# Optimization experiments

Hardware: AMD Instinct MI355X
Metric: run time of the kernel (lower is better)

Reference implementation:

```python
import jax, jax.numpy as jnp
import numpy as np

NUM_HEADS = 8


def setup_inputs() -> dict:
    key = jax.random.key(0)
    ks = jax.random.split(key, 7)
    B, C, L = 4, 512, 2048
    s = 1.0 / np.sqrt(C)
    return {
        "x": jax.random.normal(ks[0], (B, C, L), dtype=jnp.float32),
        "wq": jax.random.normal(ks[1], (C, C), dtype=jnp.float32) * s,
        "bq": jax.random.normal(ks[2], (C,), dtype=jnp.float32) * 0.01,
        "wk": jax.random.normal(ks[3], (C, C), dtype=jnp.float32) * s,
        "bk": jax.random.normal(ks[4], (C,), dtype=jnp.float32) * 0.01,
        "wv": jax.random.normal(ks[5], (C, C), dtype=jnp.float32) * s,
        "bv": jax.random.normal(ks[6], (C,), dtype=jnp.float32) * 0.01,
    }


def reference(x, wq, bq, wk, bk, wv, bv):
    B, C, L = x.shape
    H = NUM_HEADS
    Ch = C // H

    def proj(w, b):
        # 1x1 Conv1d == per-position channel GEMM: (B,C,L) x (O,C) -> (B,O,L)
        return jnp.einsum('bcl,oc->bol', x, w) + b[None, :, None]

    q = proj(wq, bq).reshape(B, H, Ch, L)
    k = proj(wk, bk).reshape(B, H, Ch, L)
    v = proj(wv, bv).reshape(B, H, Ch, L)

    # q^T k over channel dim -> (B,H,L,L)
    scale = 1.0 / jnp.sqrt(jnp.asarray(Ch, dtype=x.dtype))
    scores = jnp.einsum('bhcl,bhcm->bhlm', q, k) * scale
    attn = jax.nn.softmax(scores, axis=-1)

    # FAITHFUL quirk: torch code uses .view (reshape), NOT transpose, on v
    v2 = v.reshape(B, H, L, Ch)
    out = jnp.einsum('bhlm,bhmc->bhlc', attn, v2)
    # and .view back to (B, C, L) — again a plain reshape
    return out.reshape(B, C, L)
```

## Files before the change

### kernel.cpp

```cpp
#include <hip/hip_runtime.h>


typedef unsigned short u16;
typedef unsigned int   u32;
typedef short bf16x8 __attribute__((ext_vector_type(8)));
typedef u16  u16x8  __attribute__((ext_vector_type(8)));
typedef float f32x16 __attribute__((ext_vector_type(16)));

#define SCALE_Q 0.18033688011112042f

__device__ __forceinline__ u16 f2b(float f) {
    u32 u = __float_as_uint(f);
    u += 0x7FFFu + ((u >> 16) & 1u);
    return (u16)(u >> 16);
}

__device__ __forceinline__ float exp2_(float x) {
#if __has_builtin(__builtin_amdgcn_exp2f)
    return __builtin_amdgcn_exp2f(x);
#else
    return exp2f(x);
#endif
}

__device__ __forceinline__ u32 cvtpk(float lo, float hi) {
    u32 d;
    asm("v_cvt_pk_bf16_f32 %0, %1, %2" : "=v"(d) : "v"(lo), "v"(hi));
    return d;
}

__device__ __forceinline__ void pl32swap(u32& a, u32& b) {
    asm volatile("v_permlane32_swap_b32 %0, %1" : "+v"(a), "+v"(b));
}

__device__ __forceinline__ void g2l16(const u16* g, u16* l) {
    __builtin_amdgcn_global_load_lds(
        (const __attribute__((address_space(1))) unsigned int*)g,
        (__attribute__((address_space(3))) unsigned int*)l, 16, 0, 0);
}

#define WAITV(N) asm volatile("s_waitcnt vmcnt(" #N ")" ::: "memory")
#define WAITL0   asm volatile("s_waitcnt lgkmcnt(0)" ::: "memory")
#define SBAR     __builtin_amdgcn_s_barrier()
#define SCHED0   __builtin_amdgcn_sched_barrier(0)

__global__ __launch_bounds__(256) void prep_kernel(
    const float* __restrict__ wq, const float* __restrict__ wk,
    const float* __restrict__ wv, const float* __restrict__ x,
    u16* __restrict__ wcat, u16* __restrict__ xT)
{
    const int bid = blockIdx.x, t = threadIdx.x;
    if (bid < 384) {
        int e0 = bid * 2048 + t * 8;
        const float* src = (e0 < 262144) ? wq : (e0 < 524288) ? wk : wv;
        int eo = e0 & 262143;
        float4 a = *(const float4*)(src + eo);
        float4 b = *(const float4*)(src + eo + 4);
        u16x8 o;
        o[0]=f2b(a.x); o[1]=f2b(a.y); o[2]=f2b(a.z); o[3]=f2b(a.w);
        o[4]=f2b(b.x); o[5]=f2b(b.y); o[6]=f2b(b.z); o[7]=f2b(b.w);
        *(u16x8*)(wcat + e0) = o;
        return;
    }
    int xb = bid - 384;
    int b = xb >> 8, ct = (xb >> 5) & 7, lt = xb & 31;
    __shared__ float lds[64 * 65];
#pragma unroll
    for (int it = 0; it < 4; ++it) {
        int s = t + it * 256;
        int cr = s >> 4, l4 = (s & 15) * 4;
        float4 v = *(const float4*)(x + ((size_t)(b * 512 + ct * 64 + cr)) * 2048 + lt * 64 + l4);
        lds[(l4 + 0) * 65 + cr] = v.x;
        lds[(l4 + 1) * 65 + cr] = v.y;
        lds[(l4 + 2) * 65 + cr] = v.z;
        lds[(l4 + 3) * 65 + cr] = v.w;
    }
    __syncthreads();
    {
        int l = t >> 2, c16 = (t & 3) * 16;
        u16x8 o0, o1;
#pragma unroll
        for (int i = 0; i < 8; ++i) o0[i] = f2b(lds[l * 65 + c16 + i]);
#pragma unroll
        for (int i = 0; i < 8; ++i) o1[i] = f2b(lds[l * 65 + c16 + 8 + i]);
        u16* d = xT + ((size_t)(b * 2048 + lt * 64 + l)) * 512 + ct * 64 + c16;
        *(u16x8*)d = o0;
        *(u16x8*)(d + 8) = o1;
    }
}

__global__ __launch_bounds__(256) void proj_kernel(
    const u16* __restrict__ wcat, const u16* __restrict__ xT,
    const float* __restrict__ bq, const float* __restrict__ bk,
    const float* __restrict__ bv,
    u16* __restrict__ qt, u16* __restrict__ kt, u16* __restrict__ vv)
{
    const int d = blockIdx.x;
    const int i = d >> 3;
    const int combo = (d & 7) * 8 + i / 12;
    const int ot = i % 12;
    const int b  = combo >> 4;
    const int lt = combo & 15;
    const int l0 = lt * 128, o0 = ot * 128;
    const int sel = o0 >> 9, ol0 = o0 & 511;
    const float* __restrict__ bias = (sel == 0) ? bq : (sel == 1) ? bk : bv;

    __shared__ __align__(16) u16 wt[128 * 64];
    __shared__ __align__(16) u16 xt[128 * 64];

    const int tid = threadIdx.x, wid = tid >> 6, lane = tid & 63;
    const int hlf = lane >> 5, i32 = lane & 31;
    const int lrow = lane >> 3, lg = lane & 7;
    const int wo = wid >> 1, wl = wid & 1;

    f32x16 acc[2][2];
#pragma unroll
    for (int a = 0; a < 2; ++a)
#pragma unroll
        for (int c = 0; c < 2; ++c)
#pragma unroll
            for (int r = 0; r < 16; ++r) acc[a][c][r] = 0.f;

    for (int c0 = 0; c0 < 512; c0 += 64) {
#pragma unroll
        for (int cc = 0; cc < 4; ++cc) {
            int rb = (wid * 4 + cc) * 8;
            int rw = rb + lrow;
            int sg = (lg ^ (rw & 7)) << 3;
            g2l16(wcat + (size_t)(o0 + rw) * 512 + c0 + sg, wt + rb * 64);
            g2l16(xT + ((size_t)(b * 2048 + l0 + rw)) * 512 + c0 + sg, xt + rb * 64);
        }
        WAITV(0);
        SBAR;
        SCHED0;
        bf16x8 wf[2][4], xf[2][4];
#pragma unroll
        for (int a = 0; a < 2; ++a)
#pragma unroll
            for (int ks = 0; ks < 4; ++ks) {
                int rw = wo * 64 + a * 32 + i32;
                wf[a][ks] = *(const bf16x8*)(wt + rw * 64 + (((ks * 2 + hlf) ^ (rw & 7)) << 3));
                int rx = wl * 64 + a * 32 + i32;
                xf[a][ks] = *(const bf16x8*)(xt + rx * 64 + (((ks * 2 + hlf) ^ (rx & 7)) << 3));
            }
        if (sel < 2) {
#pragma unroll
            for (int a = 0; a < 2; ++a)
#pragma unroll
                for (int c = 0; c < 2; ++c)
#pragma unroll
                    for (int ks = 0; ks < 4; ++ks)
                        acc[a][c] = __builtin_amdgcn_mfma_f32_32x32x16_bf16(xf[a][ks], wf[c][ks], acc[a][c], 0, 0, 0);
        } else {
#pragma unroll
            for (int a = 0; a < 2; ++a)
#pragma unroll
                for (int c = 0; c < 2; ++c)
#pragma unroll
                    for (int ks = 0; ks < 4; ++ks)
                        acc[a][c] = __builtin_amdgcn_mfma_f32_32x32x16_bf16(wf[a][ks], xf[c][ks], acc[a][c], 0, 0, 0);
        }
        WAITL0;
        SCHED0;
        SBAR;
    }

    if (sel < 2) {
        u16* __restrict__ dst = (sel == 0) ? qt : kt;
        const float sc = (sel == 0) ? SCALE_Q : 1.0f;
#pragma unroll
        for (int c = 0; c < 2; ++c) {
            int cg = ol0 + wo * 64 + c * 32 + i32;
            int h = cg >> 6, c6 = cg & 63;
            float bb = bias[cg];
#pragma unroll
            for (int a = 0; a < 2; ++a)
#pragma unroll
                for (int r = 0; r < 16; ++r) {
                    int l = l0 + wl * 64 + a * 32 + (r & 3) + 8 * (r >> 2) + 4 * hlf;
                    dst[(((size_t)(b * 8 + h)) * 2048 + l) * 64 + c6] = f2b((acc[a][c][r] + bb) * sc);
                }
        }
    } else {
#pragma unroll
        for (int a = 0; a < 2; ++a)
#pragma unroll
            for (int r = 0; r < 16; ++r) {
                int ov = ol0 + wo * 64 + a * 32 + (r & 3) + 8 * (r >> 2) + 4 * hlf;
                float bb = bias[ov];
#pragma unroll
                for (int c = 0; c < 2; ++c) {
                    int l = l0 + wl * 64 + c * 32 + i32;
                    vv[((size_t)(b * 512 + ov)) * 2048 + l] = f2b(acc[a][c][r] + bb);
                }
            }
    }
}

__global__ __launch_bounds__(256) void vtrans_kernel(
    const u16* __restrict__ vv, u16* __restrict__ vtg)
{
    const int bh = blockIdx.x >> 5, mt = blockIdx.x & 31;
    const u16* __restrict__ src = vv + (size_t)bh * 131072 + mt * 4096;
    __shared__ u16 lds[64 * 65];
    const int t = threadIdx.x;
    const int m = t >> 2, c16 = (t & 3) * 16;
    u16x8 a = *(const u16x8*)(src + t * 16);
    u16x8 b = *(const u16x8*)(src + t * 16 + 8);
#pragma unroll
    for (int i = 0; i < 8; ++i) lds[(c16 + i) * 65 + m] = a[i];
#pragma unroll
    for (int i = 0; i < 8; ++i) lds[(c16 + 8 + i) * 65 + m] = b[i];
    __syncthreads();
    const int c = t >> 2, m16 = (t & 3) * 16;
    u16x8 o0, o1;
#pragma unroll
    for (int i = 0; i < 8; ++i) o0[i] = lds[c * 65 + m16 + i];
#pragma unroll
    for (int i = 0; i < 8; ++i) o1[i] = lds[c * 65 + m16 + 8 + i];
    u16* d = vtg + (size_t)bh * 131072 + (size_t)c * 2048 + mt * 64 + m16;
    *(u16x8*)d = o0;
    *(u16x8*)(d + 8) = o1;
}

__global__ __launch_bounds__(256, 4) void attn_kernel(
    const u16* __restrict__ qt, const u16* __restrict__ kt,
    const u16* __restrict__ vtg, float* __restrict__ out,
    float* __restrict__ p1a, float* __restrict__ p1b,
    float* __restrict__ ls0, float* __restrict__ ls1)
{
    const int d = blockIdx.x;
    const int w = (d & 7) * 128 + (d >> 3);
    const int lt = w & 15;
    const int g  = w >> 4;
    const int bh = g >> 1;
    const int mh = g & 1;
    const int l0 = lt * 128;
    const int tid = threadIdx.x, wid = tid >> 6, lane = tid & 63;
    const int hlf = lane >> 5, i32 = lane & 31;
    const int lrow = lane >> 3, lg = lane & 7;

    __shared__ __align__(16) u16 smem[16384];
    float* olds = (float*)smem;

    bf16x8 qf[4];
    {
        const u16* qrow = qt + ((size_t)bh * 2048 + l0 + wid * 32 + i32) * 64;
#pragma unroll
        for (int ks = 0; ks < 4; ++ks)
            qf[ks] = *(const bf16x8*)(qrow + ks * 16 + hlf * 8);
    }
    const u16* __restrict__ kb = kt + (size_t)bh * 2048 * 64;
    const u16* __restrict__ vb = vtg + (size_t)bh * 131072;

    bf16x8 ones;
#pragma unroll
    for (int i = 0; i < 8; ++i) ones[i] = (short)0x3F80;

    f32x16 oacc[2], lacc;
#pragma unroll
    for (int c = 0; c < 2; ++c)
#pragma unroll
        for (int r = 0; r < 16; ++r) oacc[c][r] = 0.f;
#pragma unroll
    for (int r = 0; r < 16; ++r) lacc[r] = 0.f;

#define STAGE(T, BUF) do {                                                        \
    if (wid < 2) {                                                                \
        _Pragma("unroll")                                                         \
        for (int cc = 0; cc < 4; ++cc) {                                          \
            int row = wid * 32 + cc * 8 + lrow;                                   \
            g2l16(kb + (size_t)((T) * 64 + row) * 64 + ((lg ^ lrow) << 3),        \
                  smem + (BUF) * 4096 + (wid * 4 + cc) * 512);                    \
        }                                                                         \
    } else {                                                                      \
        _Pragma("unroll")                                                         \
        for (int cc = 0; cc < 4; ++cc) {                                          \
            int crow = (wid - 2) * 32 + cc * 8 + lrow;                            \
            g2l16(vb + (size_t)crow * 2048 + (T) * 64 + ((lg ^ lrow) << 3),       \
                  smem + 8192 + (BUF) * 4096 + ((wid - 2) * 4 + cc) * 512);       \
        }                                                                         \
    } } while (0)

    const int t0 = mh * 16;
    STAGE(t0, 0);

    for (int t = 0; t < 16; ++t) {
        const int cb = t & 1;
        if (t < 15) {
            STAGE(t0 + t + 1, cb ^ 1);
            WAITV(4);
        } else {
            WAITV(0);
        }
        SBAR;
        SCHED0;

        const u16* kbuf = smem + cb * 4096;
        const u16* vbuf = smem + 8192 + cb * 4096;

        f32x16 st[2];
        __builtin_amdgcn_s_setprio(1);
#pragma unroll
        for (int mi = 0; mi < 2; ++mi) {
#pragma unroll
            for (int r = 0; r < 16; ++r) st[mi][r] = 0.f;
#pragma unroll
            for (int ks = 0; ks < 4; ++ks) {
                int row = mi * 32 + i32;
                bf16x8 kf = *(const bf16x8*)(kbuf + row * 64 + (((ks * 2 + hlf) ^ (row & 7)) << 3));
                st[mi] = __builtin_amdgcn_mfma_f32_32x32x16_bf16(kf, qf[ks], st[mi], 0, 0, 0);
            }
        }
        __builtin_amdgcn_s_setprio(0);

#pragma unroll
        for (int mi = 0; mi < 2; ++mi)
#pragma unroll
            for (int r = 0; r < 16; ++r)
                st[mi][r] = exp2_(st[mi][r]);

        bf16x8 pf[4];
#pragma unroll
        for (int ks = 0; ks < 4; ++ks) {
            int mi = ks >> 1, rb = (ks & 1) * 8;
            u32 A1 = cvtpk(st[mi][rb + 0], st[mi][rb + 1]);
            u32 B1 = cvtpk(st[mi][rb + 2], st[mi][rb + 3]);
            u32 A2 = cvtpk(st[mi][rb + 4], st[mi][rb + 5]);
            u32 B2 = cvtpk(st[mi][rb + 6], st[mi][rb + 7]);
            pl32swap(A1, A2);
            pl32swap(B1, B2);
            union { u32 ww[4]; bf16x8 v; } u;
            u.ww[0] = A1; u.ww[1] = B1; u.ww[2] = A2; u.ww[3] = B2;
            pf[ks] = u.v;
        }

        __builtin_amdgcn_s_setprio(1);
#pragma unroll
        for (int ci = 0; ci < 2; ++ci)
#pragma unroll
            for (int ks = 0; ks < 4; ++ks) {
                int row = ci * 32 + i32;
                bf16x8 vf = *(const bf16x8*)(vbuf + row * 64 + (((ks * 2 + hlf) ^ (row & 7)) << 3));
                oacc[ci] = __builtin_amdgcn_mfma_f32_32x32x16_bf16(vf, pf[ks], oacc[ci], 0, 0, 0);
            }
#pragma unroll
        for (int ks = 0; ks < 4; ++ks)
            lacc = __builtin_amdgcn_mfma_f32_32x32x16_bf16(ones, pf[ks], lacc, 0, 0, 0);
        __builtin_amdgcn_s_setprio(0);

        WAITL0;
        SCHED0;
        SBAR;
    }

    if (lane < 32) {
        size_t ridx = (size_t)bh * 2048 + l0 + wid * 32 + lane;
        ((mh == 0) ? ls0 : ls1)[ridx] = lacc[0];
    }

    float* dstbase = (mh == 0)
        ? (out + (size_t)bh * 131072)
        : (((bh < 16) ? p1a : p1b) + (size_t)(bh & 15) * 131072);
    int ll = wid * 32 + i32;
    SCHED0;
#pragma unroll
    for (int ci = 0; ci < 2; ++ci)
#pragma unroll
        for (int r = 0; r < 16; ++r) {
            int c = ci * 32 + (r & 3) + 8 * (r >> 2) + 4 * hlf;
            olds[ll * 64 + (c ^ ((ll & 7) << 2))] = oacc[ci][r];
        }
    __syncthreads();
    {
        int l = tid >> 1, hv = tid & 1;
        float* orow = dstbase + (size_t)(l0 + l) * 64;
#pragma unroll
        for (int i = 0; i < 8; ++i) {
            int c4 = hv * 8 + i;
            float4 v = *(const float4*)(olds + l * 64 + ((c4 ^ (l & 7)) << 2));
            *(float4*)(orow + c4 * 4) = v;
        }
    }
#undef STAGE
}

__global__ __launch_bounds__(256) void combine_kernel(
    float* __restrict__ out,
    const float* __restrict__ p1a, const float* __restrict__ p1b,
    const float* __restrict__ ls0, const float* __restrict__ ls1)
{
    int q = blockIdx.x * 256 + threadIdx.x;
    int e = q * 4;
    int row = e >> 6;
    int bh = e >> 17;
    float inv = 1.0f / (ls0[row] + ls1[row]);
    float4 a = *(const float4*)(out + e);
    const float* psrc = (bh < 16) ? p1a : p1b;
    float4 b = *(const float4*)(psrc + (e & 2097151));
    float4 r;
    r.x = (a.x + b.x) * inv;
    r.y = (a.y + b.y) * inv;
    r.z = (a.z + b.z) * inv;
    r.w = (a.w + b.w) * inv;
    *(float4*)(out + e) = r;
}

extern "C" void kernel_launch(void* const* d_in, const int* in_sizes, int n_in,
                              void* d_out, int out_size, void* d_ws, size_t ws_size,
                              hipStream_t stream) {
    const float* x  = (const float*)d_in[0];
    const float* wq = (const float*)d_in[1];
    const float* bq = (const float*)d_in[2];
    const float* wk = (const float*)d_in[3];
    const float* bk = (const float*)d_in[4];
    const float* wv = (const float*)d_in[5];
    const float* bv = (const float*)d_in[6];
    float* out = (float*)d_out;

    u16* wcat = (u16*)d_ws;
    u16* xT   = wcat + 786432;
    u16* qt   = xT + 4194304;
    u16* kt   = qt + 4194304;
    u16* vv   = kt + 4194304;
    u16* vtg  = vv + 4194304;

    float* ls0 = (float*)wcat;
    float* ls1 = ls0 + 65536;
    float* p1a = (float*)xT;
    float* p1b = (float*)vv;

    prep_kernel<<<1408, 256, 0, stream>>>(wq, wk, wv, x, wcat, xT);
    proj_kernel<<<768, 256, 0, stream>>>(wcat, xT, bq, bk, bv, qt, kt, vv);
    vtrans_kernel<<<1024, 256, 0, stream>>>(vv, vtg);
    attn_kernel<<<1024, 256, 0, stream>>>(qt, kt, vtg, out, p1a, p1b, ls0, ls1);
    combine_kernel<<<4096, 256, 0, stream>>>(out, p1a, p1b, ls0, ls1);
}
```

Before: 109.3 us.

## Load K/V fragments directly from global memory, drop LDS staging and ones-MFMA rowsum

```diff
diff --git a/kernel.cpp b/kernel.cpp
--- a/kernel.cpp
+++ b/kernel.cpp
@@ -223,7 +223,7 @@
     *(u16x8*)(d + 8) = o1;
 }
 
-__global__ __launch_bounds__(256, 4) void attn_kernel(
+__global__ __launch_bounds__(256) void attn_kernel(
     const u16* __restrict__ qt, const u16* __restrict__ kt,
     const u16* __restrict__ vtg, float* __restrict__ out,
     float* __restrict__ p1a, float* __restrict__ p1b,
@@ -238,10 +238,8 @@
     const int l0 = lt * 128;
     const int tid = threadIdx.x, wid = tid >> 6, lane = tid & 63;
     const int hlf = lane >> 5, i32 = lane & 31;
-    const int lrow = lane >> 3, lg = lane & 7;
-
-    __shared__ __align__(16) u16 smem[16384];
-    float* olds = (float*)smem;
+
+    __shared__ __align__(16) float olds[128 * 64];
 
     bf16x8 qf[4];
     {
@@ -250,75 +248,50 @@
         for (int ks = 0; ks < 4; ++ks)
             qf[ks] = *(const bf16x8*)(qrow + ks * 16 + hlf * 8);
     }
-    const u16* __restrict__ kb = kt + (size_t)bh * 2048 * 64;
-    const u16* __restrict__ vb = vtg + (size_t)bh * 131072;
-
-    bf16x8 ones;
-#pragma unroll
-    for (int i = 0; i < 8; ++i) ones[i] = (short)0x3F80;
-
-    f32x16 oacc[2], lacc;
+    const u16* __restrict__ kb = kt + ((size_t)bh * 2048 + mh * 1024 + i32) * 64 + hlf * 8;
+    const u16* __restrict__ vb = vtg + (size_t)bh * 131072 + (size_t)i32 * 2048
+                                 + mh * 1024 + hlf * 8;
+
+    float l_loc = 0.f;
+    f32x16 oacc[2];
 #pragma unroll
     for (int c = 0; c < 2; ++c)
 #pragma unroll
         for (int r = 0; r < 16; ++r) oacc[c][r] = 0.f;
-#pragma unroll
-    for (int r = 0; r < 16; ++r) lacc[r] = 0.f;
-
-#define STAGE(T, BUF) do {                                                        \
-    if (wid < 2) {                                                                \
-        _Pragma("unroll")                                                         \
-        for (int cc = 0; cc < 4; ++cc) {                                          \
-            int row = wid * 32 + cc * 8 + lrow;                                   \
-            g2l16(kb + (size_t)((T) * 64 + row) * 64 + ((lg ^ lrow) << 3),        \
-                  smem + (BUF) * 4096 + (wid * 4 + cc) * 512);                    \
-        }                                                                         \
-    } else {                                                                      \
-        _Pragma("unroll")                                                         \
-        for (int cc = 0; cc < 4; ++cc) {                                          \
-            int crow = (wid - 2) * 32 + cc * 8 + lrow;                            \
-            g2l16(vb + (size_t)crow * 2048 + (T) * 64 + ((lg ^ lrow) << 3),       \
-                  smem + 8192 + (BUF) * 4096 + ((wid - 2) * 4 + cc) * 512);       \
-        }                                                                         \
-    } } while (0)
-
-    const int t0 = mh * 16;
-    STAGE(t0, 0);
-
+
+#pragma unroll 2
     for (int t = 0; t < 16; ++t) {
-        const int cb = t & 1;
-        if (t < 15) {
-            STAGE(t0 + t + 1, cb ^ 1);
-            WAITV(4);
-        } else {
-            WAITV(0);
-        }
-        SBAR;
-        SCHED0;
-
-        const u16* kbuf = smem + cb * 4096;
-        const u16* vbuf = smem + 8192 + cb * 4096;
+        bf16x8 kf[2][4], vf[2][4];
+#pragma unroll
+        for (int mi = 0; mi < 2; ++mi)
+#pragma unroll
+            for (int ks = 0; ks < 4; ++ks)
+                kf[mi][ks] = *(const bf16x8*)(kb + ((size_t)(t * 64 + mi * 32)) * 64 + ks * 16);
+#pragma unroll
+        for (int ci = 0; ci < 2; ++ci)
+#pragma unroll
+            for (int ks = 0; ks < 4; ++ks)
+                vf[ci][ks] = *(const bf16x8*)(vb + (size_t)(ci * 32) * 2048 + t * 64 + ks * 16);
 
         f32x16 st[2];
-        __builtin_amdgcn_s_setprio(1);
 #pragma unroll
         for (int mi = 0; mi < 2; ++mi) {
 #pragma unroll
             for (int r = 0; r < 16; ++r) st[mi][r] = 0.f;
 #pragma unroll
-            for (int ks = 0; ks < 4; ++ks) {
-                int row = mi * 32 + i32;
-                bf16x8 kf = *(const bf16x8*)(kbuf + row * 64 + (((ks * 2 + hlf) ^ (row & 7)) << 3));
-                st[mi] = __builtin_amdgcn_mfma_f32_32x32x16_bf16(kf, qf[ks], st[mi], 0, 0, 0);
+            for (int ks = 0; ks < 4; ++ks)
+                st[mi] = __builtin_amdgcn_mfma_f32_32x32x16_bf16(kf[mi][ks], qf[ks], st[mi], 0, 0, 0);
+        }
+
+        float psum = 0.f;
+#pragma unroll
+        for (int mi = 0; mi < 2; ++mi)
+#pragma unroll
+            for (int r = 0; r < 16; ++r) {
+                st[mi][r] = exp2_(st[mi][r]);
+                psum += st[mi][r];
             }
-        }
-        __builtin_amdgcn_s_setprio(0);
-
-#pragma unroll
-        for (int mi = 0; mi < 2; ++mi)
-#pragma unroll
-            for (int r = 0; r < 16; ++r)
-                st[mi][r] = exp2_(st[mi][r]);
+        l_loc += psum;
 
         bf16x8 pf[4];
 #pragma unroll
@@ -335,35 +308,23 @@
             pf[ks] = u.v;
         }
 
-        __builtin_amdgcn_s_setprio(1);
 #pragma unroll
         for (int ci = 0; ci < 2; ++ci)
 #pragma unroll
-            for (int ks = 0; ks < 4; ++ks) {
-                int row = ci * 32 + i32;
-                bf16x8 vf = *(const bf16x8*)(vbuf + row * 64 + (((ks * 2 + hlf) ^ (row & 7)) << 3));
-                oacc[ci] = __builtin_amdgcn_mfma_f32_32x32x16_bf16(vf, pf[ks], oacc[ci], 0, 0, 0);
-            }
-#pragma unroll
-        for (int ks = 0; ks < 4; ++ks)
-            lacc = __builtin_amdgcn_mfma_f32_32x32x16_bf16(ones, pf[ks], lacc, 0, 0, 0);
-        __builtin_amdgcn_s_setprio(0);
-
-        WAITL0;
-        SCHED0;
-        SBAR;
-    }
-
+            for (int ks = 0; ks < 4; ++ks)
+                oacc[ci] = __builtin_amdgcn_mfma_f32_32x32x16_bf16(vf[ci][ks], pf[ks], oacc[ci], 0, 0, 0);
+    }
+
+    float lfull = l_loc + __shfl_xor(l_loc, 32);
     if (lane < 32) {
         size_t ridx = (size_t)bh * 2048 + l0 + wid * 32 + lane;
-        ((mh == 0) ? ls0 : ls1)[ridx] = lacc[0];
+        ((mh == 0) ? ls0 : ls1)[ridx] = lfull;
     }
 
     float* dstbase = (mh == 0)
         ? (out + (size_t)bh * 131072)
         : (((bh < 16) ? p1a : p1b) + (size_t)(bh & 15) * 131072);
     int ll = wid * 32 + i32;
-    SCHED0;
 #pragma unroll
     for (int ci = 0; ci < 2; ++ci)
 #pragma unroll
@@ -382,7 +343,6 @@
             *(float4*)(orow + c4 * 4) = v;
         }
     }
-#undef STAGE
 }
 
 __global__ __launch_bounds__(256) void combine_kernel(
```

After: 181.4 us. +66.0%, slower.

## Fuse split-K combine into attention via atomic ticket handoff between block pairs

Applied to the files above, without the earlier changes.

```diff
diff --git a/kernel.cpp b/kernel.cpp
--- a/kernel.cpp
+++ b/kernel.cpp
@@ -198,12 +198,15 @@
 }
 
 __global__ __launch_bounds__(256) void vtrans_kernel(
-    const u16* __restrict__ vv, u16* __restrict__ vtg)
+    const u16* __restrict__ vv, u16* __restrict__ vtg, int* __restrict__ flags)
 {
+    const int t = threadIdx.x;
+    if (blockIdx.x == 0 && t < 256) {
+        ((int4*)flags)[t] = make_int4(0, 0, 0, 0);
+    }
     const int bh = blockIdx.x >> 5, mt = blockIdx.x & 31;
     const u16* __restrict__ src = vv + (size_t)bh * 131072 + mt * 4096;
     __shared__ u16 lds[64 * 65];
-    const int t = threadIdx.x;
     const int m = t >> 2, c16 = (t & 3) * 16;
     u16x8 a = *(const u16x8*)(src + t * 16);
     u16x8 b = *(const u16x8*)(src + t * 16 + 8);
@@ -226,8 +229,8 @@
 __global__ __launch_bounds__(256, 4) void attn_kernel(
     const u16* __restrict__ qt, const u16* __restrict__ kt,
     const u16* __restrict__ vtg, float* __restrict__ out,
-    float* __restrict__ p1a, float* __restrict__ p1b,
-    float* __restrict__ ls0, float* __restrict__ ls1)
+    float* __restrict__ pb_lo, float* __restrict__ pb_hi,
+    float* __restrict__ lsb, int* __restrict__ ticket, int* __restrict__ done)
 {
     const int d = blockIdx.x;
     const int w = (d & 7) * 128 + (d >> 3);
@@ -242,6 +245,7 @@
 
     __shared__ __align__(16) u16 smem[16384];
     float* olds = (float*)smem;
+    __shared__ int role_sh;
 
     bf16x8 qf[4];
     {
@@ -354,27 +358,50 @@
         SBAR;
     }
 
-    if (lane < 32) {
-        size_t ridx = (size_t)bh * 2048 + l0 + wid * 32 + lane;
-        ((mh == 0) ? ls0 : ls1)[ridx] = lacc[0];
-    }
-
-    float* dstbase = (mh == 0)
-        ? (out + (size_t)bh * 131072)
-        : (((bh < 16) ? p1a : p1b) + (size_t)(bh & 15) * 131072);
+    const int p = lt * 32 + bh;
+    float* pbuf = (bh < 16) ? (pb_lo + (size_t)(lt * 16 + bh) * 8192)
+                            : (pb_hi + (size_t)(lt * 16 + (bh - 16)) * 8192);
+
+    if (tid == 0) role_sh = atomicAdd(&ticket[p], 1);
+    __syncthreads();
+    const int role = role_sh;
+
+    if (role == 0) {
+#pragma unroll
+        for (int ci = 0; ci < 2; ++ci)
+#pragma unroll
+            for (int r = 0; r < 16; ++r)
+                pbuf[(ci * 16 + r) * 256 + tid] = oacc[ci][r];
+        if (lane < 32)
+            lsb[p * 128 + wid * 32 + lane] = lacc[0];
+        __threadfence();
+        __syncthreads();
+        if (tid == 0) atomicExch(&done[p], 1);
+        return;
+    }
+
+    if (tid == 0) {
+        while (atomicAdd(&done[p], 0) == 0) __builtin_amdgcn_s_sleep(2);
+    }
+    __syncthreads();
+    __threadfence();
+
+    float lo = lsb[p * 128 + wid * 32 + i32];
+    float inv = 1.0f / (lacc[0] + lo);
+
     int ll = wid * 32 + i32;
-    SCHED0;
 #pragma unroll
     for (int ci = 0; ci < 2; ++ci)
 #pragma unroll
         for (int r = 0; r < 16; ++r) {
+            float m = (oacc[ci][r] + pbuf[(ci * 16 + r) * 256 + tid]) * inv;
             int c = ci * 32 + (r & 3) + 8 * (r >> 2) + 4 * hlf;
-            olds[ll * 64 + (c ^ ((ll & 7) << 2))] = oacc[ci][r];
+            olds[ll * 64 + (c ^ ((ll & 7) << 2))] = m;
         }
     __syncthreads();
     {
         int l = tid >> 1, hv = tid & 1;
-        float* orow = dstbase + (size_t)(l0 + l) * 64;
+        float* orow = out + ((size_t)bh * 2048 + l0 + l) * 64;
 #pragma unroll
         for (int i = 0; i < 8; ++i) {
             int c4 = hv * 8 + i;
@@ -383,27 +410,6 @@
         }
     }
 #undef STAGE
-}
-
-__global__ __launch_bounds__(256) void combine_kernel(
-    float* __restrict__ out,
-    const float* __restrict__ p1a, const float* __restrict__ p1b,
-    const float* __restrict__ ls0, const float* __restrict__ ls1)
-{
-    int q = blockIdx.x * 256 + threadIdx.x;
-    int e = q * 4;
-    int row = e >> 6;
-    int bh = e >> 17;
-    float inv = 1.0f / (ls0[row] + ls1[row]);
-    float4 a = *(const float4*)(out + e);
-    const float* psrc = (bh < 16) ? p1a : p1b;
-    float4 b = *(const float4*)(psrc + (e & 2097151));
-    float4 r;
-    r.x = (a.x + b.x) * inv;
-    r.y = (a.y + b.y) * inv;
-    r.z = (a.z + b.z) * inv;
-    r.w = (a.w + b.w) * inv;
-    *(float4*)(out + e) = r;
 }
 
 extern "C" void kernel_launch(void* const* d_in, const int* in_sizes, int n_in,
@@ -425,14 +431,15 @@
     u16* vv   = kt + 4194304;
     u16* vtg  = vv + 4194304;
 
-    float* ls0 = (float*)wcat;
-    float* ls1 = ls0 + 65536;
-    float* p1a = (float*)xT;
-    float* p1b = (float*)vv;
+    int*   ticket = (int*)wcat;
+    int*   done   = ticket + 512;
+    float* lsb    = (float*)(ticket + 1024);
+    float* pb_lo  = (float*)xT;
+    float* pb_hi  = (float*)vv;
 
     prep_kernel<<<1408, 256, 0, stream>>>(wq, wk, wv, x, wcat, xT);
     proj_kernel<<<768, 256, 0, stream>>>(wcat, xT, bq, bk, bv, qt, kt, vv);
-    vtrans_kernel<<<1024, 256, 0, stream>>>(vv, vtg);
-    attn_kernel<<<1024, 256, 0, stream>>>(qt, kt, vtg, out, p1a, p1b, ls0, ls1);
-    combine_kernel<<<4096, 256, 0, stream>>>(out, p1a, p1b, ls0, ls1);
-}
+    vtrans_kernel<<<1024, 256, 0, stream>>>(vv, vtg, ticket);
+    attn_kernel<<<1024, 256, 0, stream>>>(qt, kt, vtg, out, pb_lo, pb_hi,
+                                          lsb, ticket, done);
+}
```

Result: slower. 235.4 us (+115.4%).
